# Performance work log

Hardware: AMD Instinct MI355X
Metric: run time of the kernel (lower is better)

## Reference

```python
import jax, jax.numpy as jnp
import numpy as np

DIM = 2048
KV_DIM = 1024
NUM_HEADS = 16
HEAD_DIM = DIM // NUM_HEADS  # 128
EPS = 1e-6
B, LQ, LKV = 2, 4096, 1024


def _rope_cos_sin(L, d, base=10000.0):
    inv_freq = 1.0 / (base ** (np.arange(0, d, 2, dtype=np.float32) / d))  # [d/2]
    freqs = np.arange(L, dtype=np.float32)[:, None] * inv_freq[None, :]   # [L, d/2]
    emb = np.concatenate([freqs, freqs], axis=-1)                          # [L, d]
    return jnp.asarray(np.cos(emb)), jnp.asarray(np.sin(emb))


def setup_inputs() -> dict:
    key = jax.random.key(0)
    ks = jax.random.split(key, 10)
    x = jax.random.normal(ks[0], (B, LQ, DIM), dtype=jnp.float32)
    y = jax.random.normal(ks[1], (B, LKV, KV_DIM), dtype=jnp.float32)
    xc, xs = _rope_cos_sin(LQ, HEAD_DIM)
    yc, ys = _rope_cos_sin(LKV, HEAD_DIM)
    x_cos = jnp.broadcast_to(xc[None], (B, LQ, HEAD_DIM))
    x_sin = jnp.broadcast_to(xs[None], (B, LQ, HEAD_DIM))
    y_cos = jnp.broadcast_to(yc[None], (B, LKV, HEAD_DIM))
    y_sin = jnp.broadcast_to(ys[None], (B, LKV, HEAD_DIM))
    s = 0.02
    Wq = jax.random.normal(ks[2], (DIM, DIM), dtype=jnp.float32) * s
    Wk = jax.random.normal(ks[3], (DIM, KV_DIM), dtype=jnp.float32) * s
    Wv = jax.random.normal(ks[4], (DIM, KV_DIM), dtype=jnp.float32) * s
    Wo = jax.random.normal(ks[5], (DIM, DIM), dtype=jnp.float32) * s
    bq = jnp.zeros((DIM,), jnp.float32)
    bk = jnp.zeros((DIM,), jnp.float32)
    bv = jnp.zeros((DIM,), jnp.float32)
    bo = jnp.zeros((DIM,), jnp.float32)
    rmsq_w = jnp.ones((DIM,), jnp.float32)
    rmsk_w = jnp.ones((DIM,), jnp.float32)
    ln_w = jnp.ones((KV_DIM,), jnp.float32)
    ln_b = jnp.zeros((KV_DIM,), jnp.float32)
    return dict(x=x, y=y, x_cos=x_cos, x_sin=x_sin, y_cos=y_cos, y_sin=y_sin,
                Wq=Wq, bq=bq, Wk=Wk, bk=bk, Wv=Wv, bv=bv, Wo=Wo, bo=bo,
                rmsq_w=rmsq_w, rmsk_w=rmsk_w, ln_w=ln_w, ln_b=ln_b)


def _rms_norm(t, w, eps=EPS):
    return t * jax.lax.rsqrt(jnp.mean(t * t, axis=-1, keepdims=True) + eps) * w


def _layer_norm(t, w, b, eps=EPS):
    mu = jnp.mean(t, axis=-1, keepdims=True)
    var = jnp.mean(jnp.square(t - mu), axis=-1, keepdims=True)
    return (t - mu) * jax.lax.rsqrt(var + eps) * w + b


def _rotate_half(t):
    d2 = t.shape[-1] // 2
    return jnp.concatenate([-t[..., d2:], t[..., :d2]], axis=-1)


def _apply_rope(t, cos, sin):
    # t: [B, L, H, D]; cos/sin: [B, L, D] -> unsqueeze head dim (unsqueeze_dim=2)
    cos = cos[:, :, None, :]
    sin = sin[:, :, None, :]
    return t * cos + _rotate_half(t) * sin


def _block_forward(x, y, x_cos, x_sin, y_cos, y_sin,
                   Wq, bq, Wk, bk, Wv, bv, Wo, bo,
                   rmsq_w, rmsk_w, ln_w, ln_b):
    Bb, Lq, D = x.shape
    Lk = y.shape[1]
    H, Dh = NUM_HEADS, HEAD_DIM
    # y pre-norm (block-level LayerNorm)
    yn = _layer_norm(y, ln_w, ln_b)
    # projections + RMSNorm on q/k
    q = _rms_norm(x @ Wq.T + bq, rmsq_w)   # [B, Lq, D]
    k = _rms_norm(yn @ Wk.T + bk, rmsk_w)  # [B, Lk, D]
    v = yn @ Wv.T + bv                     # [B, Lk, D]
    # split heads and apply RoPE
    q = _apply_rope(q.reshape(Bb, Lq, H, Dh), x_cos, x_sin)
    k = _apply_rope(k.reshape(Bb, Lk, H, Dh), y_cos, y_sin)
    v = v.reshape(Bb, Lk, H, Dh)
    # non-causal cross attention, scale = 1/sqrt(head_dim)
    scale = 1.0 / jnp.sqrt(jnp.asarray(Dh, q.dtype))
    scores = jnp.einsum('blhd,bmhd->bhlm', q, k) * scale
    probs = jax.nn.softmax(scores, axis=-1)
    out = jnp.einsum('bhlm,bmhd->blhd', probs, v).reshape(Bb, Lq, D)
    return out @ Wo.T + bo


def reference(x, y, x_cos, x_sin, y_cos, y_sin,
              Wq, bq, Wk, bk, Wv, bv, Wo, bo,
              rmsq_w, rmsk_w, ln_w, ln_b):
    return _block_forward(x, y, x_cos, x_sin, y_cos, y_sin,
                          Wq, bq, Wk, bk, Wv, bv, Wo, bo,
                          rmsq_w, rmsk_w, ln_w, ln_b)
```

## Files before the change

kernel.cpp:

```cpp
#include <hip/hip_runtime.h>


typedef __attribute__((ext_vector_type(8))) short    short8;
typedef __attribute__((ext_vector_type(8))) unsigned short ushort8;
typedef __attribute__((ext_vector_type(4))) unsigned short ushort4v;
typedef __attribute__((ext_vector_type(4))) float    f32x4;
typedef __attribute__((ext_vector_type(2))) unsigned int uint2v;

#define DEV __device__ __forceinline__

DEV unsigned short f2bf(float f) {
  unsigned int u = __builtin_bit_cast(unsigned int, f);
  u += 0x7FFFu + ((u >> 16) & 1u);
  return (unsigned short)(u >> 16);
}
DEV float bf2f(unsigned short h) {
  return __builtin_bit_cast(float, ((unsigned int)h) << 16);
}
DEV unsigned int cvtpk_bf16(float lo, float hi) {
  unsigned int r;
  asm("v_cvt_pk_bf16_f32 %0, %1, %2" : "=v"(r) : "v"(lo), "v"(hi));
  return r;
}

DEV void gload_lds16(const void* g, void* l) {
  __builtin_amdgcn_global_load_lds(
      (const __attribute__((address_space(1))) void*)g,
      (__attribute__((address_space(3))) void*)l, 16, 0, 0);
}

__global__ __launch_bounds__(256) void cvt_kernel(const float* __restrict__ in,
                                                  unsigned short* __restrict__ out,
                                                  int n4) {
  int idx = blockIdx.x * 256 + threadIdx.x;
  int stride = gridDim.x * 256;
  for (int i = idx; i < n4; i += stride) {
    float4 v = *(const float4*)(in + (size_t)i * 4);
    ushort4v o;
    o.x = f2bf(v.x); o.y = f2bf(v.y); o.z = f2bf(v.z); o.w = f2bf(v.w);
    *(ushort4v*)(out + (size_t)i * 4) = o;
  }
}

__global__ __launch_bounds__(256) void ln_kernel(const float* __restrict__ y,
                                                 const float* __restrict__ w,
                                                 const float* __restrict__ b,
                                                 unsigned short* __restrict__ yn) {
  const int row = blockIdx.x;
  const int t = threadIdx.x;
  const float* yr = y + (size_t)row * 1024;
  float4 v = *(const float4*)(yr + t * 4);
  float s1 = v.x + v.y + v.z + v.w;
  float s2 = v.x * v.x + v.y * v.y + v.z * v.z + v.w * v.w;
#pragma unroll
  for (int m = 1; m < 64; m <<= 1) {
    s1 += __shfl_xor(s1, m);
    s2 += __shfl_xor(s2, m);
  }
  __shared__ float red[8];
  const int wave = t >> 6, lane = t & 63;
  if (lane == 0) { red[wave] = s1; red[4 + wave] = s2; }
  __syncthreads();
  s1 = red[0] + red[1] + red[2] + red[3];
  s2 = red[4] + red[5] + red[6] + red[7];
  const float mu = s1 * (1.0f / 1024.0f);
  const float var = s2 * (1.0f / 1024.0f) - mu * mu;
  const float rs = rsqrtf(var + 1e-6f);
  ushort4v o;
  o.x = f2bf((v.x - mu) * rs * w[t * 4 + 0] + b[t * 4 + 0]);
  o.y = f2bf((v.y - mu) * rs * w[t * 4 + 1] + b[t * 4 + 1]);
  o.z = f2bf((v.z - mu) * rs * w[t * 4 + 2] + b[t * 4 + 2]);
  o.w = f2bf((v.w - mu) * rs * w[t * 4 + 3] + b[t * 4 + 3]);
  *(ushort4v*)(yn + (size_t)row * 1024 + t * 4) = o;
}

__global__ __launch_bounds__(256) void gemm_bt(const unsigned short* __restrict__ A,
                                               const unsigned short* __restrict__ W,
                                               const float* __restrict__ bias,
                                               unsigned short* __restrict__ Cout,
                                               int M, int N, int K) {
  __shared__ __align__(16) char sA[128 * 128];
  __shared__ __align__(16) char sB[128 * 128];
  const int tid = threadIdx.x;
  const int wave = tid >> 6, lane = tid & 63;
  const int lg = lane >> 4, l15 = lane & 15;
  const int wr = wave >> 1, wc = wave & 1;
  const int m0 = blockIdx.y * 128;
  const int n0 = blockIdx.x * 128;
  const char* Ab = (const char*)A;
  const char* Wb = (const char*)W;
  const size_t ldab = (size_t)K * 2;

  f32x4 acc[4][4] = {};

  for (int kt = 0; kt < K; kt += 64) {
#pragma unroll
    for (int i = 0; i < 4; ++i) {
      const int p = (i * 256 + tid) * 16;
      const int row = p >> 7;
      const int si = (p & 127) ^ ((row & 7) << 4);
      gload_lds16(Ab + (size_t)(m0 + row) * ldab + (size_t)kt * 2 + si, sA + p);
    }
#pragma unroll
    for (int i = 0; i < 4; ++i) {
      const int p = (i * 256 + tid) * 16;
      const int row = p >> 7;
      const int si = (p & 127) ^ ((row & 7) << 4);
      gload_lds16(Wb + (size_t)(n0 + row) * ldab + (size_t)kt * 2 + si, sB + p);
    }
    __syncthreads();
#pragma unroll
    for (int ks = 0; ks < 2; ++ks) {
      const int kb = (ks * 32 + lg * 8) * 2;
      short8 af[4], bw[4];
#pragma unroll
      for (int mf = 0; mf < 4; ++mf) {
        const int row = wr * 64 + mf * 16 + l15;
        af[mf] = *(const short8*)(sA + row * 128 + (kb ^ ((row & 7) << 4)));
      }
#pragma unroll
      for (int nf = 0; nf < 4; ++nf) {
        const int row = wc * 64 + nf * 16 + l15;
        bw[nf] = *(const short8*)(sB + row * 128 + (kb ^ ((row & 7) << 4)));
      }
#pragma unroll
      for (int mf = 0; mf < 4; ++mf)
#pragma unroll
        for (int nf = 0; nf < 4; ++nf)
          acc[mf][nf] = __builtin_amdgcn_mfma_f32_16x16x32_bf16(af[mf], bw[nf],
                                                                acc[mf][nf], 0, 0, 0);
    }
    __syncthreads();
  }

#pragma unroll
  for (int nf = 0; nf < 4; ++nf) {
    const int n = n0 + wc * 64 + nf * 16 + l15;
    const float bv = bias[n];
#pragma unroll
    for (int mf = 0; mf < 4; ++mf) {
      const int mB = m0 + wr * 64 + mf * 16 + lg * 4;
#pragma unroll
      for (int r = 0; r < 4; ++r)
        Cout[(size_t)(mB + r) * N + n] = f2bf(acc[mf][nf][r] + bv);
    }
  }
}

template <int EPI>
__global__ __launch_bounds__(512, 2) void gemm256(const unsigned short* __restrict__ A,
                                                  const unsigned short* __restrict__ W,
                                                  const float* __restrict__ bias,
                                                  void* __restrict__ Cout,
                                                  int M, int N, int K) {
  __shared__ __align__(16) char lds[2][4][16384];
  const int tid = threadIdx.x;
  const int wave = tid >> 6, lane = tid & 63;
  const int lg = lane >> 4, l15 = lane & 15;
  const int wm = wave >> 2, wn = wave & 3;

  const int nwg = gridDim.x;
  const int wgid = (blockIdx.x & 7) * (nwg >> 3) + (blockIdx.x >> 3);
  const int nbn = N >> 8;
  const int m0 = (wgid / nbn) * 256;
  const int n0 = (wgid % nbn) * 256;

  const char* Ab = (const char*)A;
  const char* Wb = (const char*)W;
  const size_t ld = (size_t)K * 2;
  const int NT = K >> 6;
  const int NI = NT >> 1;

  const int prow = tid >> 3;
  const int psw  = ((tid * 16) & 127) ^ ((prow & 7) << 4);
  const int pdst = tid * 16;
  const char* pAg = Ab + (size_t)(m0 + prow) * ld + psw;
  const char* pBg = Wb + (size_t)(n0 + prow) * ld + psw;

  f32x4 acc[8][4] = {};
  short8 af[4][2];
  short8 bf[4][2];

#define STG(BUF, HALF, ISB, TAU) do {                                         \
    const char* _g = ((ISB) ? pBg : pAg) + (size_t)(HALF) * 128 * ld +        \
                     (size_t)(TAU) * 128;                                     \
    char* _l = lds[BUF][(ISB) * 2 + (HALF)];                                  \
    gload_lds16(_g, _l + pdst);                                               \
    gload_lds16(_g + 64 * ld, _l + pdst + 8192);                              \
  } while (0)

#define LDA(BUF, H) do {                                                      \
    const char* _b = lds[BUF][wm];                                            \
    _Pragma("unroll") for (int mfl = 0; mfl < 4; ++mfl) {                     \
      const int _r = (H) * 64 + mfl * 16 + l15;                               \
      _Pragma("unroll") for (int ks = 0; ks < 2; ++ks)                        \
        af[mfl][ks] = *(const short8*)(_b + _r * 128 +                        \
                        ((ks * 64 + lg * 16) ^ ((_r & 7) << 4)));             \
    }                                                                         \
  } while (0)

#define LDB(BUF, G) do {                                                      \
    const char* _b = lds[BUF][2 + (wn >> 1)];                                 \
    _Pragma("unroll") for (int nfl = 0; nfl < 2; ++nfl) {                     \
      const int _r = (wn & 1) * 64 + (G) * 32 + nfl * 16 + l15;               \
      _Pragma("unroll") for (int ks = 0; ks < 2; ++ks)                        \
        bf[(G) * 2 + nfl][ks] = *(const short8*)(_b + _r * 128 +              \
                        ((ks * 64 + lg * 16) ^ ((_r & 7) << 4)));             \
    }                                                                         \
  } while (0)

#define MFMA_Q(H, G) do {                                                     \
    __builtin_amdgcn_s_setprio(1);                                            \
    _Pragma("unroll") for (int ks = 0; ks < 2; ++ks)                          \
    _Pragma("unroll") for (int mfl = 0; mfl < 4; ++mfl)                       \
    _Pragma("unroll") for (int nfl = 0; nfl < 2; ++nfl)                       \
      acc[(H) * 4 + mfl][(G) * 2 + nfl] =                                     \
        __builtin_amdgcn_mfma_f32_16x16x32_bf16(af[mfl][ks],                  \
            bf[(G) * 2 + nfl][ks], acc[(H) * 4 + mfl][(G) * 2 + nfl], 0,0,0); \
    __builtin_amdgcn_s_setprio(0);                                            \
  } while (0)

#define BAR() __builtin_amdgcn_s_barrier()
#define LGKM0() do { asm volatile("s_waitcnt lgkmcnt(0)" ::: "memory");       \
    __builtin_amdgcn_sched_barrier(0); } while (0)
#define VM4() asm volatile("s_waitcnt vmcnt(4)" ::: "memory")
#define VM0() asm volatile("s_waitcnt vmcnt(0)" ::: "memory")

  STG(0, 0, 0, 0); STG(0, 1, 0, 0); STG(0, 0, 1, 0); STG(0, 1, 1, 0);
  STG(1, 0, 1, 1); STG(1, 1, 1, 1);
  VM4(); BAR();

  for (int t = 0; t < NI - 1; ++t) {
    const int t2 = 2 * t;
    LDA(0, 0); LDB(0, 0); STG(1, 0, 0, t2 + 1);
    BAR(); LGKM0(); MFMA_Q(0, 0); BAR();
    LDB(0, 1); STG(1, 1, 0, t2 + 1);
    BAR(); LGKM0(); MFMA_Q(0, 1); BAR();
    LDA(0, 1); STG(0, 0, 1, t2 + 2);
    BAR(); LGKM0(); MFMA_Q(1, 1); BAR();
    STG(0, 1, 1, t2 + 2);
    BAR(); MFMA_Q(1, 0); VM4(); BAR();
    LDA(1, 0); LDB(1, 0); STG(0, 0, 0, t2 + 2);
    BAR(); LGKM0(); MFMA_Q(0, 0); BAR();
    LDB(1, 1); STG(0, 1, 0, t2 + 2);
    BAR(); LGKM0(); MFMA_Q(0, 1); BAR();
    LDA(1, 1); STG(1, 0, 1, t2 + 3);
    BAR(); LGKM0(); MFMA_Q(1, 1); BAR();
    STG(1, 1, 1, t2 + 3);
    BAR(); MFMA_Q(1, 0); VM4(); BAR();
  }

  LDA(0, 0); LDB(0, 0); STG(1, 0, 0, NT - 1);
  BAR(); LGKM0(); MFMA_Q(0, 0); BAR();
  LDB(0, 1); STG(1, 1, 0, NT - 1);
  BAR(); LGKM0(); MFMA_Q(0, 1); BAR();
  LDA(0, 1);
  BAR(); LGKM0(); MFMA_Q(1, 1); BAR();
  BAR(); MFMA_Q(1, 0); VM0(); BAR();
  LDA(1, 0); LDB(1, 0); LGKM0(); MFMA_Q(0, 0);
  LDB(1, 1); LGKM0(); MFMA_Q(0, 1);
  LDA(1, 1); LGKM0(); MFMA_Q(1, 1);
  MFMA_Q(1, 0);

#undef STG
#undef LDA
#undef LDB
#undef MFMA_Q
#undef BAR
#undef LGKM0
#undef VM4
#undef VM0

#pragma unroll
  for (int nf = 0; nf < 4; ++nf) {
    const int n = n0 + wn * 64 + nf * 16 + l15;
    const float bv = bias[n];
#pragma unroll
    for (int mf = 0; mf < 8; ++mf) {
      const int mB = m0 + wm * 128 + mf * 16 + lg * 4;
#pragma unroll
      for (int r = 0; r < 4; ++r) {
        const float v = acc[mf][nf][r] + bv;
        if constexpr (EPI == 0)
          ((unsigned short*)Cout)[(size_t)(mB + r) * N + n] = f2bf(v);
        else
          ((float*)Cout)[(size_t)(mB + r) * N + n] = v;
      }
    }
  }
}

__global__ __launch_bounds__(256) void rmsrope_kernel(const unsigned short* __restrict__ in,
                                                      const float* __restrict__ w,
                                                      const float* __restrict__ cs,
                                                      const float* __restrict__ sn,
                                                      unsigned short* __restrict__ out,
                                                      int L, float scale) {
  const int row = blockIdx.x;
  const int t = threadIdx.x;
  __shared__ __align__(16) unsigned short srow[2048];
  __shared__ float red[4];
  const unsigned short* ir = in + (size_t)row * 2048;
  ushort8 v = *(const ushort8*)(ir + t * 8);
  float vals[8];
  float ss = 0.f;
#pragma unroll
  for (int j = 0; j < 8; ++j) { vals[j] = bf2f(v[j]); ss += vals[j] * vals[j]; }
  *(ushort8*)(srow + t * 8) = v;
#pragma unroll
  for (int m = 1; m < 64; m <<= 1) ss += __shfl_xor(ss, m);
  const int wave = t >> 6, lane = t & 63;
  if (lane == 0) red[wave] = ss;
  __syncthreads();
  const float tot = red[0] + red[1] + red[2] + red[3];
  const float rms = rsqrtf(tot * (1.0f / 2048.0f) + 1e-6f);

  const int n0 = t * 8;
  const int d0 = n0 & 127;
  const int hh = n0 >> 7;
  const float sign = (d0 < 64) ? -1.0f : 1.0f;
  const float* cb = cs + (size_t)row * 128 + d0;
  const float* sb = sn + (size_t)row * 128 + d0;
  ushort8 po = *(const ushort8*)(srow + (n0 ^ 64));
  ushort8 ou;
#pragma unroll
  for (int j = 0; j < 8; ++j) {
    const float self = vals[j] * rms * w[n0 + j];
    const float part = bf2f(po[j]) * rms * w[(n0 ^ 64) + j];
    ou[j] = f2bf((self * cb[j] + sign * part * sb[j]) * scale);
  }
  const int b = row / L, l = row - (row / L) * L;
  *(ushort8*)(out + (((size_t)(b * 16 + hh)) * L + l) * 128 + d0) = ou;
}

__global__ __launch_bounds__(256) void vtrans_kernel(const unsigned short* __restrict__ vpre,
                                                     unsigned short* __restrict__ vt) {
  const int bid = blockIdx.x;
  const int kt = bid & 15, bh = bid >> 4;
  const int h = bh & 15, b = bh >> 4;
  __shared__ unsigned short lt[64][130];
  const int t = threadIdx.x;
  const int i0 = t >> 4, c0 = (t & 15) * 8;
  const unsigned short* src = vpre + ((size_t)(b * 1024 + kt * 64)) * 2048 + h * 128;
#pragma unroll
  for (int ii = 0; ii < 4; ++ii) {
    const int i = i0 + ii * 16;
    ushort8 v = *(const ushort8*)(src + (size_t)i * 2048 + c0);
#pragma unroll
    for (int j = 0; j < 8; ++j) lt[i][c0 + j] = v[j];
  }
  __syncthreads();
  const int d0 = t >> 3, j0 = (t & 7) * 8;
  unsigned short* dst = vt + (size_t)bh * 128 * 1024 + kt * 64;
#pragma unroll
  for (int dd = 0; dd < 4; ++dd) {
    const int d = d0 + dd * 32;
    ushort8 o;
#pragma unroll
    for (int jj = 0; jj < 8; ++jj) o[jj] = lt[j0 + jj][d];
    *(ushort8*)(dst + (size_t)d * 1024 + j0) = o;
  }
}

__global__ __launch_bounds__(512, 2) void attn_kernel(const unsigned short* __restrict__ q,
                                                      const unsigned short* __restrict__ k,
                                                      const unsigned short* __restrict__ vt,
                                                      unsigned short* __restrict__ ao) {
  __shared__ __align__(16) char sK[2][64 * 256];
  __shared__ __align__(16) char sV[2][128 * 128];
  __shared__ __align__(16) char sP[8][32 * 128];

  const int bid = blockIdx.x;
  const int qt = bid & 15, bh = bid >> 4;
  const int tid = threadIdx.x;
  const int wave = tid >> 6, lane = tid & 63;
  const int lg = lane >> 4, l15 = lane & 15;

  const unsigned short* qbase = q + (((size_t)bh * 4096) + qt * 256 + wave * 32) * 128;
  const char* kbase = (const char*)(k + (size_t)bh * 1024 * 128);
  const char* vbase = (const char*)(vt + (size_t)bh * 128 * 1024);

  short8 qa[2][4];
#pragma unroll
  for (int mf = 0; mf < 2; ++mf)
#pragma unroll
    for (int ks = 0; ks < 4; ++ks)
      qa[mf][ks] = *(const short8*)(qbase + (size_t)(mf * 16 + l15) * 128 + ks * 32 + lg * 8);

  f32x4 o[2][8] = {};
  float lsum[2] = {0.f, 0.f};
  char* const pb = sP[wave];

#define STAGE_KV(BUF, KV0) do {                                              \
    _Pragma("unroll")                                                        \
    for (int i = 0; i < 2; ++i) {                                            \
      const int p = (i * 512 + tid) * 16;                                    \
      const int row = p >> 8;                                                \
      const int si = (p & 255) ^ ((row & 7) << 4);                           \
      gload_lds16(kbase + (size_t)((KV0) + row) * 256 + si, sK[BUF] + p);    \
    }                                                                        \
    _Pragma("unroll")                                                        \
    for (int i = 0; i < 2; ++i) {                                            \
      const int p = (i * 512 + tid) * 16;                                    \
      const int row = p >> 7;                                                \
      const int si = (p & 127) ^ ((row & 7) << 4);                           \
      gload_lds16(vbase + (size_t)row * 2048 + (KV0) * 2 + si, sV[BUF] + p); \
    }                                                                        \
  } while (0)

  STAGE_KV(0, 0);
  __syncthreads();

  int cur = 0;
  for (int kt = 0; kt < 16; ++kt) {
    if (kt < 15) STAGE_KV(cur ^ 1, (kt + 1) * 64);

    const char* const K = sK[cur];
    const char* const V = sV[cur];

    f32x4 s[4][2] = {};
#pragma unroll
    for (int ks = 0; ks < 4; ++ks) {
      const int kb = ks * 64 + lg * 16;
#pragma unroll
      for (int f = 0; f < 4; ++f) {
        const int row = f * 16 + l15;
        short8 kf = *(const short8*)(K + row * 256 + (kb ^ ((row & 7) << 4)));
#pragma unroll
        for (int mf = 0; mf < 2; ++mf)
          s[f][mf] = __builtin_amdgcn_mfma_f32_16x16x32_bf16(kf, qa[mf][ks], s[f][mf], 0, 0, 0);
      }
    }

#pragma unroll
    for (int mf = 0; mf < 2; ++mf) {
      const int prow = mf * 16 + l15;
      const int swz = (prow & 7) << 4;
#pragma unroll
      for (int f = 0; f < 4; ++f) {
        const float p0 = exp2f(s[f][mf][0]);
        const float p1 = exp2f(s[f][mf][1]);
        const float p2 = exp2f(s[f][mf][2]);
        const float p3 = exp2f(s[f][mf][3]);
        lsum[mf] += (p0 + p1) + (p2 + p3);
        uint2v pw;
        pw.x = cvtpk_bf16(p0, p1);
        pw.y = cvtpk_bf16(p2, p3);
        *(uint2v*)(pb + prow * 128 + ((32 * f + 8 * lg) ^ swz)) = pw;
      }
    }

#pragma unroll
    for (int ks2 = 0; ks2 < 2; ++ks2) {
      const int jb = ks2 * 64 + lg * 16;
      short8 pa[2];
#pragma unroll
      for (int mf = 0; mf < 2; ++mf) {
        const int prow = mf * 16 + l15;
        pa[mf] = *(const short8*)(pb + prow * 128 + (jb ^ ((prow & 7) << 4)));
      }
#pragma unroll
      for (int nf = 0; nf < 8; ++nf) {
        const int vrow = nf * 16 + l15;
        short8 vf = *(const short8*)(V + vrow * 128 + (jb ^ ((vrow & 7) << 4)));
#pragma unroll
        for (int mf = 0; mf < 2; ++mf)
          o[mf][nf] = __builtin_amdgcn_mfma_f32_16x16x32_bf16(pa[mf], vf, o[mf][nf], 0, 0, 0);
      }
    }
    __syncthreads();
    cur ^= 1;
  }
#undef STAGE_KV

  float linv[2];
#pragma unroll
  for (int mf = 0; mf < 2; ++mf) {
    float t = lsum[mf];
    t += __shfl_xor(t, 16);
    t += __shfl_xor(t, 32);
    linv[mf] = 1.0f / t;
  }
  const int b = bh >> 4, h = bh & 15;
#pragma unroll
  for (int mf = 0; mf < 2; ++mf) {
#pragma unroll
    for (int r = 0; r < 4; ++r) {
      const float inv = __shfl(linv[mf], (lane & 48) | (lg * 4 + r));
      const int qg = qt * 256 + wave * 32 + mf * 16 + lg * 4 + r;
      const size_t orow = ((size_t)b * 4096 + qg) * 2048 + h * 128;
#pragma unroll
      for (int nf = 0; nf < 8; ++nf)
        ao[orow + nf * 16 + l15] = f2bf(o[mf][nf][r] * inv);
    }
  }
}

extern "C" void kernel_launch(void* const* d_in, const int* in_sizes, int n_in,
                              void* d_out, int out_size, void* d_ws, size_t ws_size,
                              hipStream_t stream) {
  (void)in_sizes; (void)n_in; (void)out_size; (void)ws_size;
  const float* x      = (const float*)d_in[0];
  const float* y      = (const float*)d_in[1];
  const float* x_cos  = (const float*)d_in[2];
  const float* x_sin  = (const float*)d_in[3];
  const float* y_cos  = (const float*)d_in[4];
  const float* y_sin  = (const float*)d_in[5];
  const float* Wq     = (const float*)d_in[6];
  const float* bq     = (const float*)d_in[7];
  const float* Wk     = (const float*)d_in[8];
  const float* bk     = (const float*)d_in[9];
  const float* Wv     = (const float*)d_in[10];
  const float* bv     = (const float*)d_in[11];
  const float* Wo     = (const float*)d_in[12];
  const float* bo     = (const float*)d_in[13];
  const float* rmsq_w = (const float*)d_in[14];
  const float* rmsk_w = (const float*)d_in[15];
  const float* ln_w   = (const float*)d_in[16];
  const float* ln_b   = (const float*)d_in[17];

  char* ws = (char*)d_ws;
  unsigned short* xb   = (unsigned short*)(ws + 0);
  unsigned short* Wqb  = (unsigned short*)(ws + 33554432);
  unsigned short* Wkb  = (unsigned short*)(ws + 41943040);
  unsigned short* Wvb  = (unsigned short*)(ws + 46137344);
  unsigned short* Wob  = (unsigned short*)(ws + 50331648);
  unsigned short* ynb  = (unsigned short*)(ws + 58720256);
  unsigned short* kpre = (unsigned short*)(ws + 62914560);
  unsigned short* vpre = (unsigned short*)(ws + 71303168);
  unsigned short* qpre = (unsigned short*)(ws + 62914560);
  unsigned short* qr   = (unsigned short*)(ws + 96468992);
  unsigned short* kr   = (unsigned short*)(ws + 130023424);
  unsigned short* vt   = (unsigned short*)(ws + 138412032);
  unsigned short* ao   = xb;

  const float qscale = 1.4426950408889634f * 0.08838834764831843f;

  cvt_kernel<<<2048, 256, 0, stream>>>(x, xb, (2 * 4096 * 2048) / 4);
  cvt_kernel<<<512, 256, 0, stream>>>(Wq, Wqb, (2048 * 2048) / 4);
  cvt_kernel<<<512, 256, 0, stream>>>(Wk, Wkb, (2048 * 1024) / 4);
  cvt_kernel<<<512, 256, 0, stream>>>(Wv, Wvb, (2048 * 1024) / 4);
  cvt_kernel<<<512, 256, 0, stream>>>(Wo, Wob, (2048 * 2048) / 4);
  ln_kernel<<<2048, 256, 0, stream>>>(y, ln_w, ln_b, ynb);

  dim3 gKV(16, 16);
  gemm_bt<<<gKV, 256, 0, stream>>>(ynb, Wkb, bk, kpre, 2048, 2048, 1024);
  gemm_bt<<<gKV, 256, 0, stream>>>(ynb, Wvb, bv, vpre, 2048, 2048, 1024);
  rmsrope_kernel<<<2048, 256, 0, stream>>>(kpre, rmsk_w, y_cos, y_sin, kr, 1024, 1.0f);
  vtrans_kernel<<<512, 256, 0, stream>>>(vpre, vt);

  gemm256<0><<<256, 512, 0, stream>>>(xb, Wqb, bq, qpre, 8192, 2048, 2048);
  rmsrope_kernel<<<8192, 256, 0, stream>>>(qpre, rmsq_w, x_cos, x_sin, qr, 4096, qscale);

  attn_kernel<<<512, 512, 0, stream>>>(qr, kr, vt, ao);

  gemm256<1><<<256, 512, 0, stream>>>(ao, Wob, bo, (float*)d_out, 8192, 2048, 2048);
}
```

Before: 342.2 us.

## Fuse K and V projections into one GEMM and split attention P tile in halves

The K and V projection GEMMs now run as a single launch over a concatenated weight (Wk followed by Wv in the workspace), writing an interleaved [rows, 4096] output with a per-column bias select. The rmsrope and V-transpose kernels take a leading-dimension argument so they can read from that combined buffer. The attention inner loop handles the 64-key tile as two 32-key halves, which halves the per-wave P scratch in LDS and interleaves the QK, softmax and PV work. The fusion saves one launch and fills the GPU better on a small GEMM, while the LDS reduction may allow higher occupancy or shorten register live ranges.

```diff
diff --git a/kernel.cpp b/kernel.cpp
--- a/kernel.cpp
+++ b/kernel.cpp
@@ -76,7 +76,9 @@
 
 __global__ __launch_bounds__(256) void gemm_bt(const unsigned short* __restrict__ A,
                                                const unsigned short* __restrict__ W,
-                                               const float* __restrict__ bias,
+                                               const float* __restrict__ bias0,
+                                               const float* __restrict__ bias1,
+                                               int nsplit,
                                                unsigned short* __restrict__ Cout,
                                                int M, int N, int K) {
   __shared__ __align__(16) char sA[128 * 128];
@@ -136,7 +138,7 @@
 #pragma unroll
   for (int nf = 0; nf < 4; ++nf) {
     const int n = n0 + wc * 64 + nf * 16 + l15;
-    const float bv = bias[n];
+    const float bv = (n < nsplit) ? bias0[n] : bias1[n - nsplit];
 #pragma unroll
     for (int mf = 0; mf < 4; ++mf) {
       const int mB = m0 + wr * 64 + mf * 16 + lg * 4;
@@ -295,12 +297,12 @@
                                                       const float* __restrict__ cs,
                                                       const float* __restrict__ sn,
                                                       unsigned short* __restrict__ out,
-                                                      int L, float scale) {
+                                                      int L, int ldin, float scale) {
   const int row = blockIdx.x;
   const int t = threadIdx.x;
   __shared__ __align__(16) unsigned short srow[2048];
   __shared__ float red[4];
-  const unsigned short* ir = in + (size_t)row * 2048;
+  const unsigned short* ir = in + (size_t)row * ldin;
   ushort8 v = *(const ushort8*)(ir + t * 8);
   float vals[8];
   float ss = 0.f;
@@ -334,18 +336,19 @@
 }
 
 __global__ __launch_bounds__(256) void vtrans_kernel(const unsigned short* __restrict__ vpre,
-                                                     unsigned short* __restrict__ vt) {
+                                                     unsigned short* __restrict__ vt,
+                                                     int ldv) {
   const int bid = blockIdx.x;
   const int kt = bid & 15, bh = bid >> 4;
   const int h = bh & 15, b = bh >> 4;
   __shared__ unsigned short lt[64][130];
   const int t = threadIdx.x;
   const int i0 = t >> 4, c0 = (t & 15) * 8;
-  const unsigned short* src = vpre + ((size_t)(b * 1024 + kt * 64)) * 2048 + h * 128;
+  const unsigned short* src = vpre + ((size_t)(b * 1024 + kt * 64)) * ldv + h * 128;
 #pragma unroll
   for (int ii = 0; ii < 4; ++ii) {
     const int i = i0 + ii * 16;
-    ushort8 v = *(const ushort8*)(src + (size_t)i * 2048 + c0);
+    ushort8 v = *(const ushort8*)(src + (size_t)i * ldv + c0);
 #pragma unroll
     for (int j = 0; j < 8; ++j) lt[i][c0 + j] = v[j];
   }
@@ -368,7 +371,7 @@
                                                       unsigned short* __restrict__ ao) {
   __shared__ __align__(16) char sK[2][64 * 256];
   __shared__ __align__(16) char sV[2][128 * 128];
-  __shared__ __align__(16) char sP[8][32 * 128];
+  __shared__ __align__(16) char sP[8][32 * 64];
 
   const int bid = blockIdx.x;
   const int qt = bid & 15, bh = bid >> 4;
@@ -418,47 +421,48 @@
     const char* const K = sK[cur];
     const char* const V = sV[cur];
 
-    f32x4 s[4][2] = {};
-#pragma unroll
-    for (int ks = 0; ks < 4; ++ks) {
-      const int kb = ks * 64 + lg * 16;
-#pragma unroll
-      for (int f = 0; f < 4; ++f) {
-        const int row = f * 16 + l15;
-        short8 kf = *(const short8*)(K + row * 256 + (kb ^ ((row & 7) << 4)));
-#pragma unroll
-        for (int mf = 0; mf < 2; ++mf)
-          s[f][mf] = __builtin_amdgcn_mfma_f32_16x16x32_bf16(kf, qa[mf][ks], s[f][mf], 0, 0, 0);
-      }
-    }
-
-#pragma unroll
-    for (int mf = 0; mf < 2; ++mf) {
-      const int prow = mf * 16 + l15;
-      const int swz = (prow & 7) << 4;
-#pragma unroll
-      for (int f = 0; f < 4; ++f) {
-        const float p0 = exp2f(s[f][mf][0]);
-        const float p1 = exp2f(s[f][mf][1]);
-        const float p2 = exp2f(s[f][mf][2]);
-        const float p3 = exp2f(s[f][mf][3]);
-        lsum[mf] += (p0 + p1) + (p2 + p3);
-        uint2v pw;
-        pw.x = cvtpk_bf16(p0, p1);
-        pw.y = cvtpk_bf16(p2, p3);
-        *(uint2v*)(pb + prow * 128 + ((32 * f + 8 * lg) ^ swz)) = pw;
-      }
-    }
-
-#pragma unroll
-    for (int ks2 = 0; ks2 < 2; ++ks2) {
-      const int jb = ks2 * 64 + lg * 16;
-      short8 pa[2];
+#pragma unroll
+    for (int hf = 0; hf < 2; ++hf) {
+      f32x4 s[2][2] = {};
+#pragma unroll
+      for (int ks = 0; ks < 4; ++ks) {
+        const int kb = ks * 64 + lg * 16;
+#pragma unroll
+        for (int fl = 0; fl < 2; ++fl) {
+          const int krow = hf * 32 + fl * 16 + l15;
+          short8 kf = *(const short8*)(K + krow * 256 + (kb ^ ((krow & 7) << 4)));
+#pragma unroll
+          for (int mf = 0; mf < 2; ++mf)
+            s[fl][mf] = __builtin_amdgcn_mfma_f32_16x16x32_bf16(kf, qa[mf][ks],
+                                                                s[fl][mf], 0, 0, 0);
+        }
+      }
+
 #pragma unroll
       for (int mf = 0; mf < 2; ++mf) {
         const int prow = mf * 16 + l15;
-        pa[mf] = *(const short8*)(pb + prow * 128 + (jb ^ ((prow & 7) << 4)));
-      }
+        const int swz = (prow & 3) << 4;
+#pragma unroll
+        for (int fl = 0; fl < 2; ++fl) {
+          const float p0 = exp2f(s[fl][mf][0]);
+          const float p1 = exp2f(s[fl][mf][1]);
+          const float p2 = exp2f(s[fl][mf][2]);
+          const float p3 = exp2f(s[fl][mf][3]);
+          lsum[mf] += (p0 + p1) + (p2 + p3);
+          uint2v pw;
+          pw.x = cvtpk_bf16(p0, p1);
+          pw.y = cvtpk_bf16(p2, p3);
+          *(uint2v*)(pb + prow * 64 + ((32 * fl + 8 * lg) ^ swz)) = pw;
+        }
+      }
+
+      short8 pa[2];
+#pragma unroll
+      for (int mf = 0; mf < 2; ++mf) {
+        const int prow = mf * 16 + l15;
+        pa[mf] = *(const short8*)(pb + prow * 64 + ((lg * 16) ^ ((prow & 3) << 4)));
+      }
+      const int jb = hf * 64 + lg * 16;
 #pragma unroll
       for (int nf = 0; nf < 8; ++nf) {
         const int vrow = nf * 16 + l15;
@@ -520,19 +524,18 @@
   const float* ln_b   = (const float*)d_in[17];
 
   char* ws = (char*)d_ws;
-  unsigned short* xb   = (unsigned short*)(ws + 0);
-  unsigned short* Wqb  = (unsigned short*)(ws + 33554432);
-  unsigned short* Wkb  = (unsigned short*)(ws + 41943040);
-  unsigned short* Wvb  = (unsigned short*)(ws + 46137344);
-  unsigned short* Wob  = (unsigned short*)(ws + 50331648);
-  unsigned short* ynb  = (unsigned short*)(ws + 58720256);
-  unsigned short* kpre = (unsigned short*)(ws + 62914560);
-  unsigned short* vpre = (unsigned short*)(ws + 71303168);
-  unsigned short* qpre = (unsigned short*)(ws + 62914560);
-  unsigned short* qr   = (unsigned short*)(ws + 96468992);
-  unsigned short* kr   = (unsigned short*)(ws + 130023424);
-  unsigned short* vt   = (unsigned short*)(ws + 138412032);
-  unsigned short* ao   = xb;
+  unsigned short* xb    = (unsigned short*)(ws + 0);
+  unsigned short* Wqb   = (unsigned short*)(ws + 33554432);
+  unsigned short* Wkb   = (unsigned short*)(ws + 41943040);
+  unsigned short* Wvb   = (unsigned short*)(ws + 46137344);
+  unsigned short* Wob   = (unsigned short*)(ws + 50331648);
+  unsigned short* ynb   = (unsigned short*)(ws + 58720256);
+  unsigned short* kvpre = (unsigned short*)(ws + 62914560);
+  unsigned short* qpre  = (unsigned short*)(ws + 62914560);
+  unsigned short* qr    = (unsigned short*)(ws + 96468992);
+  unsigned short* kr    = (unsigned short*)(ws + 130023424);
+  unsigned short* vt    = (unsigned short*)(ws + 138412032);
+  unsigned short* ao    = xb;
 
   const float qscale = 1.4426950408889634f * 0.08838834764831843f;
 
@@ -543,14 +546,13 @@
   cvt_kernel<<<512, 256, 0, stream>>>(Wo, Wob, (2048 * 2048) / 4);
   ln_kernel<<<2048, 256, 0, stream>>>(y, ln_w, ln_b, ynb);
 
-  dim3 gKV(16, 16);
-  gemm_bt<<<gKV, 256, 0, stream>>>(ynb, Wkb, bk, kpre, 2048, 2048, 1024);
-  gemm_bt<<<gKV, 256, 0, stream>>>(ynb, Wvb, bv, vpre, 2048, 2048, 1024);
-  rmsrope_kernel<<<2048, 256, 0, stream>>>(kpre, rmsk_w, y_cos, y_sin, kr, 1024, 1.0f);
-  vtrans_kernel<<<512, 256, 0, stream>>>(vpre, vt);
+  dim3 gKV(32, 16);
+  gemm_bt<<<gKV, 256, 0, stream>>>(ynb, Wkb, bk, bv, 2048, kvpre, 2048, 4096, 1024);
+  rmsrope_kernel<<<2048, 256, 0, stream>>>(kvpre, rmsk_w, y_cos, y_sin, kr, 1024, 4096, 1.0f);
+  vtrans_kernel<<<512, 256, 0, stream>>>(kvpre + 2048, vt, 4096);
 
   gemm256<0><<<256, 512, 0, stream>>>(xb, Wqb, bq, qpre, 8192, 2048, 2048);
-  rmsrope_kernel<<<8192, 256, 0, stream>>>(qpre, rmsq_w, x_cos, x_sin, qr, 4096, qscale);
+  rmsrope_kernel<<<8192, 256, 0, stream>>>(qpre, rmsq_w, x_cos, x_sin, qr, 4096, 2048, qscale);
 
   attn_kernel<<<512, 512, 0, stream>>>(qr, kr, vt, ao);
 
```

Measured after the change: 329.5 us. -3.7%, faster.
